# Kernel optimization log

Measured on AMD Instinct MI355X. Metric: run time of the kernel, lower is better.

Reference implementation:

```python
import jax, jax.numpy as jnp
import numpy as np

N_NODES = 50000
N_EDGES = 600000
IN_DIM = 128
HID = 128
OUT_DIM = 2
N_GRAPHS = 64
EPS = 1e-12  # F.normalize default eps


def setup_inputs() -> dict:
    key = jax.random.key(0)
    ks = jax.random.split(key, 16)
    s = 0.05
    x = jax.random.normal(ks[0], (N_NODES, IN_DIM), jnp.float32)
    edge_index = jax.random.randint(ks[1], (2, N_EDGES), 0, N_NODES, dtype=jnp.int32)
    batch = jnp.sort(jax.random.randint(ks[2], (N_NODES,), 0, N_GRAPHS, dtype=jnp.int32))
    # GraphSage layer 0: lin (IN->HID), agg_lin (IN+HID -> HID)
    lin_w0 = jax.random.normal(ks[3], (IN_DIM, HID), jnp.float32) * s
    lin_b0 = jnp.zeros((HID,), jnp.float32)
    agg_w0 = jax.random.normal(ks[4], (HID + IN_DIM, HID), jnp.float32) * s
    agg_b0 = jnp.zeros((HID,), jnp.float32)
    # GraphSage layer 1: lin (HID->HID), agg_lin (2*HID -> HID)
    lin_w1 = jax.random.normal(ks[5], (HID, HID), jnp.float32) * s
    lin_b1 = jnp.zeros((HID,), jnp.float32)
    agg_w1 = jax.random.normal(ks[6], (2 * HID, HID), jnp.float32) * s
    agg_b1 = jnp.zeros((HID,), jnp.float32)
    # post_mp: Linear(HID,HID) -> Dropout -> Linear(HID,OUT)
    mp_w1 = jax.random.normal(ks[7], (HID, HID), jnp.float32) * s
    mp_b1 = jnp.zeros((HID,), jnp.float32)
    mp_w2 = jax.random.normal(ks[8], (HID, OUT_DIM), jnp.float32) * s
    mp_b2 = jnp.zeros((OUT_DIM,), jnp.float32)
    return dict(x=x, edge_index=edge_index, batch=batch,
                lin_w0=lin_w0, lin_b0=lin_b0, agg_w0=agg_w0, agg_b0=agg_b0,
                lin_w1=lin_w1, lin_b1=lin_b1, agg_w1=agg_w1, agg_b1=agg_b1,
                mp_w1=mp_w1, mp_b1=mp_b1, mp_w2=mp_w2, mp_b2=mp_b2)


def sage_layer(x, lin_w, lin_b, agg_w, agg_b, src, dst, num_nodes):
    # message: ReLU(Linear(x_j)) gathered along source nodes  [E, HID]
    msg = jax.nn.relu(x[src] @ lin_w + lin_b)
    # aggr='mean' scatter to target nodes
    summed = jax.ops.segment_sum(msg, dst, num_segments=num_nodes)
    deg = jax.ops.segment_sum(jnp.ones((src.shape[0], 1), x.dtype), dst,
                              num_segments=num_nodes)
    agg = summed / jnp.maximum(deg, 1.0)
    # update: ReLU(Linear([aggr, x])) then L2-normalize rows
    h = jax.nn.relu(jnp.concatenate([agg, x], axis=-1) @ agg_w + agg_b)
    norm = jnp.sqrt(jnp.sum(h * h, axis=1, keepdims=True))
    return h / jnp.maximum(norm, EPS)


def reference(x, edge_index, batch,
              lin_w0, lin_b0, agg_w0, agg_b0,
              lin_w1, lin_b1, agg_w1, agg_b1,
              mp_w1, mp_b1, mp_w2, mp_b2):
    src, dst = edge_index[0], edge_index[1]
    n = x.shape[0]
    h = sage_layer(x, lin_w0, lin_b0, agg_w0, agg_b0, src, dst, n)
    # F.relu is a no-op on the non-negative normalized output; dropout p=0 -> identity
    h = sage_layer(h, lin_w1, lin_b1, agg_w1, agg_b1, src, dst, n)
    # global max pool over graphs
    pooled = jax.ops.segment_max(h, batch, num_segments=N_GRAPHS)
    pooled = jnp.where(jnp.isfinite(pooled), pooled, 0.0)  # guard empty graphs
    # post_mp: Linear -> Dropout(identity) -> Linear
    z = (pooled @ mp_w1 + mp_b1) @ mp_w2 + mp_b2
    return jax.nn.log_softmax(z, axis=1)
```

## Files before the change

kernel.cpp:

```cpp
#include <hip/hip_runtime.h>

__device__ __forceinline__ float bf2f(ushort u) {
    union { uint i; float f; } c; c.i = ((uint)u) << 16; return c.f;
}
__device__ __forceinline__ float bf2lo(uint v) {
    union { uint i; float f; } c; c.i = v << 16; return c.f;
}
__device__ __forceinline__ float bf2hi(uint v) {
    union { uint i; float f; } c; c.i = v & 0xffff0000u; return c.f;
}
__device__ __forceinline__ ushort f2bf(float f) {
    union { float f; uint i; } c; c.f = f;
    uint b = c.i;
    uint r = (b + 0x7fffu + ((b >> 16) & 1u)) >> 16;
    return (ushort)r;
}

typedef __bf16 v8bf __attribute__((ext_vector_type(8)));
typedef float  v4f  __attribute__((ext_vector_type(4)));

__global__ __launch_bounds__(256) void sniff_kernel(const uint* __restrict__ words, int* __restrict__ flag) {
    __shared__ int s[256];
    int t = threadIdx.x;
    int bad = 0;
    for (int i = t; i < 2048; i += 256) {
        uint w = words[i];
        uint exp = (w >> 7) & 0xffu;
        if (exp >= 143u) bad++;
    }
    s[t] = bad;
    __syncthreads();
    for (int o = 128; o; o >>= 1) {
        if (t < o) s[t] += s[t + o];
        __syncthreads();
    }
    if (t == 0) *flag = (s[0] > 64) ? 1 : 0;
}

__device__ __forceinline__ ushort load_conv(const void* src, int i, int isf32) {
    return isf32 ? f2bf(((const float*)src)[i]) : ((const ushort*)src)[i];
}

__global__ __launch_bounds__(256) void convert_x8(const void* __restrict__ src, ushort* __restrict__ dst,
                                                  int n, const int* __restrict__ flag) {
    int idx = blockIdx.x * 256 + threadIdx.x;
    int base = idx * 8;
    if (base + 8 <= n) {
        if (*flag) {
            const float4* s4 = (const float4*)src;
            float4 a = s4[idx * 2], b = s4[idx * 2 + 1];
            union { ushort u[8]; uint4 v; } o;
            o.u[0] = f2bf(a.x); o.u[1] = f2bf(a.y); o.u[2] = f2bf(a.z); o.u[3] = f2bf(a.w);
            o.u[4] = f2bf(b.x); o.u[5] = f2bf(b.y); o.u[6] = f2bf(b.z); o.u[7] = f2bf(b.w);
            *(uint4*)(dst + base) = o.v;
        } else {
            *(uint4*)(dst + base) = ((const uint4*)src)[idx];
        }
    } else {
        int isf = *flag;
        for (int i = base; i < n; i++) dst[i] = load_conv(src, i, isf);
    }
}

struct SmallSrcs { const void* p[8]; };
__global__ __launch_bounds__(256) void prep_weights(
    const void* __restrict__ w0, const void* __restrict__ wa0,
    const void* __restrict__ w1, const void* __restrict__ wa1,
    ushort* __restrict__ t0, ushort* __restrict__ ta0,
    ushort* __restrict__ t1, ushort* __restrict__ ta1,
    SmallSrcs s, ushort* __restrict__ smalldst,
    const int* __restrict__ flag) {
    int idx = blockIdx.x * 256 + threadIdx.x;
    if (idx < 98304) {
        const void* W; ushort* T; int K; int local;
        if (idx < 16384)      { W = w0;  T = t0;  K = 128; local = idx; }
        else if (idx < 49152) { W = wa0; T = ta0; K = 256; local = idx - 16384; }
        else if (idx < 65536) { W = w1;  T = t1;  K = 128; local = idx - 49152; }
        else                  { W = wa1; T = ta1; K = 256; local = idx - 65536; }
        ushort v = load_conv(W, local, *flag);
        int k = local >> 7;
        int n = local & 127;
        T[(size_t)n * K + k] = v;
    } else {
        int si = idx - 98304;
        if (si >= 17282) return;
        const int offs[9] = {0, 128, 256, 384, 512, 16896, 17024, 17280, 17282};
        int seg = 0;
        while (si >= offs[seg + 1]) seg++;
        smalldst[si] = load_conv(s.p[seg], si - offs[seg], *flag);
    }
}

__global__ __launch_bounds__(256) void count_deg(const int* __restrict__ dst, int* __restrict__ deg, int E) {
    int i = blockIdx.x * 256 + threadIdx.x;
    if (i < E) atomicAdd(&deg[dst[i]], 1);
}

#define SCAN_CHUNK 1024

__global__ __launch_bounds__(256) void chunk_sum_kernel(const int* __restrict__ deg,
                                                        int* __restrict__ csums, int n) {
    __shared__ int s[256];
    int t = threadIdx.x;
    int base = blockIdx.x * SCAN_CHUNK + t * 4;
    int v = 0;
    if (base + 4 <= n) {
        int4 q = *(const int4*)(deg + base);
        v = q.x + q.y + q.z + q.w;
    } else {
        for (int i = base; i < n; i++) v += deg[i];
    }
    s[t] = v;
    __syncthreads();
    for (int o = 128; o; o >>= 1) {
        if (t < o) s[t] += s[t + o];
        __syncthreads();
    }
    if (t == 0) csums[blockIdx.x] = s[0];
}

__global__ __launch_bounds__(256) void scan_phase2(const int* __restrict__ deg,
                                                   const int* __restrict__ csums,
                                                   int* __restrict__ rowptr, int* __restrict__ cursor,
                                                   int n) {
    __shared__ int red[256];
    int t = threadIdx.x, b = blockIdx.x;
    int v = 0;
    for (int i = t; i < b; i += 256) v += csums[i];
    red[t] = v;
    __syncthreads();
    for (int o = 128; o; o >>= 1) {
        if (t < o) red[t] += red[t + o];
        __syncthreads();
    }
    int chunkOff = red[0];
    __syncthreads();
    int base = b * SCAN_CHUNK + t * 4;
    int d0 = 0, d1 = 0, d2 = 0, d3 = 0;
    if (base + 4 <= n) {
        int4 q = *(const int4*)(deg + base);
        d0 = q.x; d1 = q.y; d2 = q.z; d3 = q.w;
    } else {
        if (base < n)     d0 = deg[base];
        if (base + 1 < n) d1 = deg[base + 1];
        if (base + 2 < n) d2 = deg[base + 2];
        if (base + 3 < n) d3 = deg[base + 3];
    }
    int s4 = d0 + d1 + d2 + d3;
    red[t] = s4;
    __syncthreads();
    for (int o = 1; o < 256; o <<= 1) {
        int u = (t >= o) ? red[t - o] : 0;
        __syncthreads();
        red[t] += u;
        __syncthreads();
    }
    int run = chunkOff + red[t] - s4;
    if (base < n)     { rowptr[base]     = run; cursor[base]     = run; run += d0; }
    if (base + 1 < n) { rowptr[base + 1] = run; cursor[base + 1] = run; run += d1; }
    if (base + 2 < n) { rowptr[base + 2] = run; cursor[base + 2] = run; run += d2; }
    if (base + 3 < n) { rowptr[base + 3] = run; cursor[base + 3] = run; run += d3; }
    if (n >= base && n < base + 4) rowptr[n] = run;
}

__global__ __launch_bounds__(256) void fill_kernel(const int* __restrict__ src, const int* __restrict__ dst,
                                                   int* __restrict__ cursor, int* __restrict__ csr_src, int E) {
    int i = blockIdx.x * 256 + threadIdx.x;
    if (i < E) {
        int pos = atomicAdd(&cursor[dst[i]], 1);
        csr_src[pos] = src[i];
    }
}

template <int NSTAGE, bool NORM, bool POOL>
__global__ __launch_bounds__(256) void gemm_kernel(
    const ushort* __restrict__ A0, const ushort* __restrict__ A1,
    const ushort* __restrict__ Bt, const ushort* __restrict__ bias,
    ushort* __restrict__ Cout, int M,
    const int* __restrict__ batchv, int* __restrict__ pooled) {
    __shared__ __bf16 As[128 * 72];
    __shared__ __bf16 Bs[128 * 72];
    __shared__ int PoolLoc[POOL ? 8 * 128 : 1];
    const int t = threadIdx.x;
    const int w = t >> 6, lane = t & 63, ln = lane & 15, q = lane >> 4;
    const int blockRow = blockIdx.x * 128;
    const int K = NSTAGE * 128;

    if (POOL) {
        for (int i = t; i < 8 * 128; i += 256) PoolLoc[i] = 0;
    }

    v4f acc[2][8];
#pragma unroll
    for (int i = 0; i < 2; i++)
#pragma unroll
        for (int j = 0; j < 8; j++) acc[i][j] = (v4f){0.f, 0.f, 0.f, 0.f};

    for (int kc = 0; kc < K; kc += 64) {
        const ushort* Ap = (kc < 128) ? A0 : A1;
        int kin = kc & 127;
#pragma unroll
        for (int i = 0; i < 4; i++) {
            int c = i * 256 + t;
            int row = c >> 3, c8 = c & 7;
            int grow = blockRow + row; if (grow >= M) grow = M - 1;
            *(uint4*)&As[row * 72 + c8 * 8] = *(const uint4*)(Ap + (size_t)grow * 128 + kin + c8 * 8);
            *(uint4*)&Bs[row * 72 + c8 * 8] = *(const uint4*)(Bt + (size_t)row * K + kc + c8 * 8);
        }
        __syncthreads();
#pragma unroll
        for (int k0 = 0; k0 < 64; k0 += 32) {
            v8bf a0 = *(const v8bf*)&As[(w * 32 + ln) * 72 + k0 + q * 8];
            v8bf a1 = *(const v8bf*)&As[(w * 32 + 16 + ln) * 72 + k0 + q * 8];
#pragma unroll
            for (int nt = 0; nt < 8; nt++) {
                v8bf b = *(const v8bf*)&Bs[(nt * 16 + ln) * 72 + k0 + q * 8];
                acc[0][nt] = __builtin_amdgcn_mfma_f32_16x16x32_bf16(a0, b, acc[0][nt], 0, 0, 0);
                acc[1][nt] = __builtin_amdgcn_mfma_f32_16x16x32_bf16(a1, b, acc[1][nt], 0, 0, 0);
            }
        }
        __syncthreads();
    }

    float biasf[8];
#pragma unroll
    for (int nt = 0; nt < 8; nt++) biasf[nt] = bf2f(bias[nt * 16 + ln]);

    const int minB = POOL ? batchv[blockRow < M ? blockRow : M - 1] : 0;

#pragma unroll
    for (int mt = 0; mt < 2; mt++) {
        float v[8][4];
#pragma unroll
        for (int nt = 0; nt < 8; nt++)
#pragma unroll
            for (int r = 0; r < 4; r++) {
                float x = acc[mt][nt][r] + biasf[nt];
                v[nt][r] = x > 0.f ? x : 0.f;
            }
        float inv[4];
        if (NORM) {
#pragma unroll
            for (int r = 0; r < 4; r++) {
                float p = 0.f;
#pragma unroll
                for (int nt = 0; nt < 8; nt++) p += v[nt][r] * v[nt][r];
                p += __shfl_xor(p, 1);
                p += __shfl_xor(p, 2);
                p += __shfl_xor(p, 4);
                p += __shfl_xor(p, 8);
                inv[r] = 1.0f / fmaxf(sqrtf(p), 1e-12f);
            }
        }
        int rowbase = blockRow + w * 32 + mt * 16 + q * 4;
#pragma unroll
        for (int r = 0; r < 4; r++) {
            int grow = rowbase + r;
            if (grow < M) {
                if (POOL) {
                    int b = batchv[grow];
                    int rel = b - minB;
#pragma unroll
                    for (int nt = 0; nt < 8; nt++) {
                        float x = v[nt][r] * inv[r];
                        int xi = __float_as_int(x);
                        if (rel < 8) atomicMax(&PoolLoc[rel * 128 + nt * 16 + ln], xi);
                        else         atomicMax(&pooled[b * 128 + nt * 16 + ln], xi);
                    }
                } else {
#pragma unroll
                    for (int nt = 0; nt < 8; nt++) {
                        float x = NORM ? v[nt][r] * inv[r] : v[nt][r];
                        Cout[(size_t)grow * 128 + nt * 16 + ln] = f2bf(x);
                    }
                }
            }
        }
    }

    if (POOL) {
        __syncthreads();
        int lastRow = blockRow + 127; if (lastRow >= M) lastRow = M - 1;
        int span = batchv[lastRow] - minB + 1;
        if (span > 8) span = 8;
        for (int i = t; i < span * 128; i += 256) {
            int vv = PoolLoc[i];
            if (vv != 0) atomicMax(&pooled[(minB + (i >> 7)) * 128 + (i & 127)], vv);
        }
    }
}

__global__ __launch_bounds__(256) void aggregate_kernel(
    const ushort* __restrict__ msg, const int* __restrict__ rowptr,
    const int* __restrict__ csr_src, ushort* __restrict__ agg, int n) {
    int wid = (int)((blockIdx.x * 256u + threadIdx.x) >> 6);
    int lane = threadIdx.x & 63;
    int sub = lane >> 4;
    int l16 = lane & 15;
    if (wid >= n) return;
    int start = rowptr[wid], end = rowptr[wid + 1];
    float a[8] = {0.f, 0.f, 0.f, 0.f, 0.f, 0.f, 0.f, 0.f};
#pragma unroll 2
    for (int j = start + sub; j < end; j += 4) {
        int s = csr_src[j];
        uint4 v = *(const uint4*)(msg + (size_t)s * 128 + l16 * 8);
        a[0] += bf2lo(v.x); a[1] += bf2hi(v.x);
        a[2] += bf2lo(v.y); a[3] += bf2hi(v.y);
        a[4] += bf2lo(v.z); a[5] += bf2hi(v.z);
        a[6] += bf2lo(v.w); a[7] += bf2hi(v.w);
    }
#pragma unroll
    for (int i = 0; i < 8; i++) {
        a[i] += __shfl_xor(a[i], 16);
        a[i] += __shfl_xor(a[i], 32);
    }
    if (sub == 0) {
        float inv = 1.0f / fmaxf((float)(end - start), 1.0f);
        union { ushort u[8]; uint4 v; } o;
#pragma unroll
        for (int i = 0; i < 8; i++) o.u[i] = f2bf(a[i] * inv);
        *(uint4*)(agg + (size_t)wid * 128 + l16 * 8) = o.v;
    }
}

__global__ __launch_bounds__(256) void final_kernel(const float* __restrict__ pooled,
                                                    const ushort* __restrict__ small,
                                                    void* __restrict__ out, int G,
                                                    const int* __restrict__ flag) {
    __shared__ float P[128];
    __shared__ float Thalf[128];
    __shared__ float T[128];
    __shared__ float R0[128], R1[128];
    const ushort* w1 = small + 512;
    const ushort* b1 = small + 16896;
    const ushort* w2 = small + 17024;
    const ushort* b2 = small + 17280;
    int g = blockIdx.x;
    int t = threadIdx.x;
    int j = t & 127, half = t >> 7;
    if (t < 128) P[t] = pooled[g * 128 + t];
    __syncthreads();
    float acc = 0.f;
    int k0 = half * 64;
#pragma unroll 8
    for (int k = k0; k < k0 + 64; k++) acc += P[k] * bf2f(w1[k * 128 + j]);
    if (half == 0) Thalf[j] = acc;
    __syncthreads();
    if (half == 1) T[j] = Thalf[j] + acc + bf2f(b1[j]);
    __syncthreads();
    if (t < 128) {
        float tv = T[t];
        R0[t] = tv * bf2f(w2[t * 2]);
        R1[t] = tv * bf2f(w2[t * 2 + 1]);
    }
    __syncthreads();
    for (int o = 64; o; o >>= 1) {
        if (t < o) { R0[t] += R0[t + o]; R1[t] += R1[t + o]; }
        __syncthreads();
    }
    if (t == 0) {
        float z0 = R0[0] + bf2f(b2[0]);
        float z1 = R1[0] + bf2f(b2[1]);
        float m = fmaxf(z0, z1);
        float l = m + logf(expf(z0 - m) + expf(z1 - m));
        float o0 = z0 - l, o1 = z1 - l;
        if (*flag) {
            ((float*)out)[2 * g]     = o0;
            ((float*)out)[2 * g + 1] = o1;
        } else {
            ((ushort*)out)[2 * g]     = f2bf(o0);
            ((ushort*)out)[2 * g + 1] = f2bf(o1);
        }
    }
}

extern "C" void kernel_launch(void* const* d_in, const int* in_sizes, int n_in,
                              void* d_out, int out_size, void* d_ws, size_t ws_size,
                              hipStream_t stream) {
    const void* x      = d_in[0];
    const int*  ei     = (const int*)d_in[1];
    const int*  batch  = (const int*)d_in[2];

    const int N = in_sizes[0] / 128;
    const int E = in_sizes[1] / 2;
    const int G = out_size / 2;
    const int* srcIdx = ei;
    const int* dstIdx = ei + E;

    char* ws = (char*)d_ws;
    size_t off = 0;
    auto alloc = [&](size_t bytes) -> void* {
        off = (off + 255) & ~(size_t)255;
        void* p = ws + off;
        off += bytes;
        return p;
    };
    int*    flag    = (int*)alloc(4);
    int*    deg     = (int*)alloc((size_t)N * 4);
    int*    rowptr  = (int*)alloc((size_t)(N + 1) * 4);
    int*    cursor  = (int*)alloc((size_t)N * 4);
    int*    csr_src = (int*)alloc((size_t)E * 4);
    int*    csums   = (int*)alloc(((size_t)N / SCAN_CHUNK + 2) * 4);
    ushort* Wt0     = (ushort*)alloc(128 * 128 * 2);
    ushort* WtA0    = (ushort*)alloc(256 * 128 * 2);
    ushort* Wt1     = (ushort*)alloc(128 * 128 * 2);
    ushort* WtA1    = (ushort*)alloc(256 * 128 * 2);
    ushort* small   = (ushort*)alloc(17282 * 2);
    ushort* xb      = (ushort*)alloc((size_t)N * 128 * 2);
    ushort* msg     = (ushort*)alloc((size_t)N * 128 * 2);
    ushort* agg     = (ushort*)alloc((size_t)N * 128 * 2);
    ushort* h0      = (ushort*)alloc((size_t)N * 128 * 2);
    int*    pooled  = (int*)alloc((size_t)G * 128 * 4);

    sniff_kernel<<<1, 256, 0, stream>>>((const uint*)x, flag);
    convert_x8<<<(N * 128 + 2047) / 2048, 256, 0, stream>>>(x, xb, N * 128, flag);
    SmallSrcs ss;
    ss.p[0] = d_in[4];  ss.p[1] = d_in[6];  ss.p[2] = d_in[8];  ss.p[3] = d_in[10];
    ss.p[4] = d_in[11]; ss.p[5] = d_in[12]; ss.p[6] = d_in[13]; ss.p[7] = d_in[14];
    prep_weights<<<452, 256, 0, stream>>>(d_in[3], d_in[5], d_in[7], d_in[9],
                                          Wt0, WtA0, Wt1, WtA1, ss, small, flag);

    hipMemsetAsync(deg, 0, (size_t)N * 4, stream);
    hipMemsetAsync(pooled, 0, (size_t)G * 128 * 4, stream);
    int eb = (E + 255) / 256;
    count_deg<<<eb, 256, 0, stream>>>(dstIdx, deg, E);
    int nchunks = (N + SCAN_CHUNK - 1) / SCAN_CHUNK;
    chunk_sum_kernel<<<nchunks, 256, 0, stream>>>(deg, csums, N);
    scan_phase2<<<N / SCAN_CHUNK + 1, 256, 0, stream>>>(deg, csums, rowptr, cursor, N);
    fill_kernel<<<eb, 256, 0, stream>>>(srcIdx, dstIdx, cursor, csr_src, E);

    int gb = (N + 127) / 128;
    int ab = (N + 3) / 4;

    gemm_kernel<1, false, false><<<gb, 256, 0, stream>>>(xb, xb, Wt0, small + 0, msg, N, nullptr, nullptr);
    aggregate_kernel<<<ab, 256, 0, stream>>>(msg, rowptr, csr_src, agg, N);
    gemm_kernel<2, true, false><<<gb, 256, 0, stream>>>(agg, xb, WtA0, small + 128, h0, N, nullptr, nullptr);

    gemm_kernel<1, false, false><<<gb, 256, 0, stream>>>(h0, h0, Wt1, small + 256, msg, N, nullptr, nullptr);
    aggregate_kernel<<<ab, 256, 0, stream>>>(msg, rowptr, csr_src, agg, N);
    gemm_kernel<2, true, true><<<gb, 256, 0, stream>>>(agg, h0, WtA1, small + 384, nullptr, N, batch, pooled);

    final_kernel<<<G, 256, 0, stream>>>((const float*)pooled, small, d_out, G, flag);
}
```

Before: 282.7 us.

## Fuse layer-1 message GEMM into layer-0 update GEMM and merge prep kernels

```diff
diff --git a/kernel.cpp b/kernel.cpp
--- a/kernel.cpp
+++ b/kernel.cpp
@@ -41,53 +41,63 @@
     return isf32 ? f2bf(((const float*)src)[i]) : ((const ushort*)src)[i];
 }
 
-__global__ __launch_bounds__(256) void convert_x8(const void* __restrict__ src, ushort* __restrict__ dst,
-                                                  int n, const int* __restrict__ flag) {
-    int idx = blockIdx.x * 256 + threadIdx.x;
-    int base = idx * 8;
-    if (base + 8 <= n) {
-        if (*flag) {
-            const float4* s4 = (const float4*)src;
-            float4 a = s4[idx * 2], b = s4[idx * 2 + 1];
-            union { ushort u[8]; uint4 v; } o;
-            o.u[0] = f2bf(a.x); o.u[1] = f2bf(a.y); o.u[2] = f2bf(a.z); o.u[3] = f2bf(a.w);
-            o.u[4] = f2bf(b.x); o.u[5] = f2bf(b.y); o.u[6] = f2bf(b.z); o.u[7] = f2bf(b.w);
-            *(uint4*)(dst + base) = o.v;
-        } else {
-            *(uint4*)(dst + base) = ((const uint4*)src)[idx];
-        }
-    } else {
-        int isf = *flag;
-        for (int i = base; i < n; i++) dst[i] = load_conv(src, i, isf);
-    }
-}
-
 struct SmallSrcs { const void* p[8]; };
-__global__ __launch_bounds__(256) void prep_weights(
+__global__ __launch_bounds__(256) void phaseA(
+    const void* __restrict__ x, ushort* __restrict__ xb, int nx, int nbconv,
     const void* __restrict__ w0, const void* __restrict__ wa0,
     const void* __restrict__ w1, const void* __restrict__ wa1,
     ushort* __restrict__ t0, ushort* __restrict__ ta0,
     ushort* __restrict__ t1, ushort* __restrict__ ta1,
     SmallSrcs s, ushort* __restrict__ smalldst,
+    int* __restrict__ deg, int* __restrict__ pooled, int N, int G,
     const int* __restrict__ flag) {
-    int idx = blockIdx.x * 256 + threadIdx.x;
-    if (idx < 98304) {
-        const void* W; ushort* T; int K; int local;
-        if (idx < 16384)      { W = w0;  T = t0;  K = 128; local = idx; }
-        else if (idx < 49152) { W = wa0; T = ta0; K = 256; local = idx - 16384; }
-        else if (idx < 65536) { W = w1;  T = t1;  K = 128; local = idx - 49152; }
-        else                  { W = wa1; T = ta1; K = 256; local = idx - 65536; }
-        ushort v = load_conv(W, local, *flag);
-        int k = local >> 7;
-        int n = local & 127;
-        T[(size_t)n * K + k] = v;
+    int b = blockIdx.x, t = threadIdx.x;
+    if (b < nbconv) {
+        int idx = b * 256 + t;
+        int base = idx * 8;
+        if (base + 8 <= nx) {
+            if (*flag) {
+                const float4* s4 = (const float4*)x;
+                float4 a = s4[idx * 2], bb = s4[idx * 2 + 1];
+                union { ushort u[8]; uint4 v; } o;
+                o.u[0] = f2bf(a.x); o.u[1] = f2bf(a.y); o.u[2] = f2bf(a.z); o.u[3] = f2bf(a.w);
+                o.u[4] = f2bf(bb.x); o.u[5] = f2bf(bb.y); o.u[6] = f2bf(bb.z); o.u[7] = f2bf(bb.w);
+                *(uint4*)(xb + base) = o.v;
+            } else {
+                *(uint4*)(xb + base) = ((const uint4*)x)[idx];
+            }
+        } else {
+            int isf = *flag;
+            for (int i = base; i < nx; i++) xb[i] = load_conv(x, i, isf);
+        }
+    } else if (b < nbconv + 452) {
+        int idx = (b - nbconv) * 256 + t;
+        if (idx < 98304) {
+            const void* W; ushort* T; int K; int local;
+            if (idx < 16384)      { W = w0;  T = t0;  K = 128; local = idx; }
+            else if (idx < 49152) { W = wa0; T = ta0; K = 256; local = idx - 16384; }
+            else if (idx < 65536) { W = w1;  T = t1;  K = 128; local = idx - 49152; }
+            else                  { W = wa1; T = ta1; K = 256; local = idx - 65536; }
+            ushort v = load_conv(W, local, *flag);
+            int k = local >> 7;
+            int n = local & 127;
+            T[(size_t)n * K + k] = v;
+        } else {
+            int si = idx - 98304;
+            if (si < 17282) {
+                const int offs[9] = {0, 128, 256, 384, 512, 16896, 17024, 17280, 17282};
+                int seg = 0;
+                while (si >= offs[seg + 1]) seg++;
+                smalldst[si] = load_conv(s.p[seg], si - offs[seg], *flag);
+            }
+        }
     } else {
-        int si = idx - 98304;
-        if (si >= 17282) return;
-        const int offs[9] = {0, 128, 256, 384, 512, 16896, 17024, 17280, 17282};
-        int seg = 0;
-        while (si >= offs[seg + 1]) seg++;
-        smalldst[si] = load_conv(s.p[seg], si - offs[seg], *flag);
+        int idx = (b - nbconv - 452) * 256 + t;
+        int nd4 = N >> 2;
+        int4 z = {0, 0, 0, 0};
+        if (idx < nd4) ((int4*)deg)[idx] = z;
+        else if (idx == nd4) { for (int i = nd4 * 4; i < N; i++) deg[i] = 0; }
+        else if (idx - nd4 - 1 < G * 32) ((int4*)pooled)[idx - nd4 - 1] = z;
     }
 }
 
@@ -172,15 +182,19 @@
     }
 }
 
-template <int NSTAGE, bool NORM, bool POOL>
+template <int NSTAGE, bool NORM, bool POOL, bool FUSE>
 __global__ __launch_bounds__(256) void gemm_kernel(
     const ushort* __restrict__ A0, const ushort* __restrict__ A1,
     const ushort* __restrict__ Bt, const ushort* __restrict__ bias,
     ushort* __restrict__ Cout, int M,
-    const int* __restrict__ batchv, int* __restrict__ pooled) {
-    __shared__ __bf16 As[128 * 72];
-    __shared__ __bf16 Bs[128 * 72];
+    const int* __restrict__ batchv, int* __restrict__ pooled,
+    const ushort* __restrict__ Bt2, const ushort* __restrict__ bias2,
+    ushort* __restrict__ Mout) {
+    constexpr int LDSN = FUSE ? (128 * 136 + 128 * 72) : (2 * 128 * 72);
+    __shared__ __bf16 lds[LDSN];
     __shared__ int PoolLoc[POOL ? 8 * 128 : 1];
+    __bf16* As = lds;
+    __bf16* Bs = lds + 128 * 72;
     const int t = threadIdx.x;
     const int w = t >> 6, lane = t & 63, ln = lane & 15, q = lane >> 4;
     const int blockRow = blockIdx.x * 128;
@@ -227,6 +241,8 @@
     for (int nt = 0; nt < 8; nt++) biasf[nt] = bf2f(bias[nt * 16 + ln]);
 
     const int minB = POOL ? batchv[blockRow < M ? blockRow : M - 1] : 0;
+    __bf16* Hs = lds;
+    ushort* HsU = (ushort*)Hs;
 
 #pragma unroll
     for (int mt = 0; mt < 2; mt++) {
@@ -252,12 +268,12 @@
                 inv[r] = 1.0f / fmaxf(sqrtf(p), 1e-12f);
             }
         }
-        int rowbase = blockRow + w * 32 + mt * 16 + q * 4;
+        int rowloc = w * 32 + mt * 16 + q * 4;
 #pragma unroll
         for (int r = 0; r < 4; r++) {
-            int grow = rowbase + r;
-            if (grow < M) {
-                if (POOL) {
+            int grow = blockRow + rowloc + r;
+            if (POOL) {
+                if (grow < M) {
                     int b = batchv[grow];
                     int rel = b - minB;
 #pragma unroll
@@ -267,12 +283,14 @@
                         if (rel < 8) atomicMax(&PoolLoc[rel * 128 + nt * 16 + ln], xi);
                         else         atomicMax(&pooled[b * 128 + nt * 16 + ln], xi);
                     }
-                } else {
-#pragma unroll
-                    for (int nt = 0; nt < 8; nt++) {
-                        float x = NORM ? v[nt][r] * inv[r] : v[nt][r];
-                        Cout[(size_t)grow * 128 + nt * 16 + ln] = f2bf(x);
-                    }
+                }
+            } else {
+#pragma unroll
+                for (int nt = 0; nt < 8; nt++) {
+                    float x = NORM ? v[nt][r] * inv[r] : v[nt][r];
+                    ushort xb = f2bf(x);
+                    if (grow < M) Cout[(size_t)grow * 128 + nt * 16 + ln] = xb;
+                    if (FUSE) HsU[(rowloc + r) * 136 + nt * 16 + ln] = xb;
                 }
             }
         }
@@ -286,6 +304,56 @@
         for (int i = t; i < span * 128; i += 256) {
             int vv = PoolLoc[i];
             if (vv != 0) atomicMax(&pooled[(minB + (i >> 7)) * 128 + (i & 127)], vv);
+        }
+    }
+
+    if (FUSE) {
+        __bf16* Bs2 = lds + 128 * 136;
+        v4f acc2[2][8];
+#pragma unroll
+        for (int i = 0; i < 2; i++)
+#pragma unroll
+            for (int j = 0; j < 8; j++) acc2[i][j] = (v4f){0.f, 0.f, 0.f, 0.f};
+
+        for (int kc = 0; kc < 128; kc += 64) {
+#pragma unroll
+            for (int i = 0; i < 4; i++) {
+                int c = i * 256 + t;
+                int row = c >> 3, c8 = c & 7;
+                *(uint4*)&Bs2[row * 72 + c8 * 8] = *(const uint4*)(Bt2 + (size_t)row * 128 + kc + c8 * 8);
+            }
+            __syncthreads();
+#pragma unroll
+            for (int k0 = 0; k0 < 64; k0 += 32) {
+                v8bf a0 = *(const v8bf*)&Hs[(w * 32 + ln) * 136 + kc + k0 + q * 8];
+                v8bf a1 = *(const v8bf*)&Hs[(w * 32 + 16 + ln) * 136 + kc + k0 + q * 8];
+#pragma unroll
+                for (int nt = 0; nt < 8; nt++) {
+                    v8bf b = *(const v8bf*)&Bs2[(nt * 16 + ln) * 72 + k0 + q * 8];
+                    acc2[0][nt] = __builtin_amdgcn_mfma_f32_16x16x32_bf16(a0, b, acc2[0][nt], 0, 0, 0);
+                    acc2[1][nt] = __builtin_amdgcn_mfma_f32_16x16x32_bf16(a1, b, acc2[1][nt], 0, 0, 0);
+                }
+            }
+            __syncthreads();
+        }
+
+        float biasf2[8];
+#pragma unroll
+        for (int nt = 0; nt < 8; nt++) biasf2[nt] = bf2f(bias2[nt * 16 + ln]);
+#pragma unroll
+        for (int mt = 0; mt < 2; mt++) {
+            int rowbase = blockRow + w * 32 + mt * 16 + q * 4;
+#pragma unroll
+            for (int r = 0; r < 4; r++) {
+                int grow = rowbase + r;
+                if (grow < M) {
+#pragma unroll
+                    for (int nt = 0; nt < 8; nt++) {
+                        float x = acc2[mt][nt][r] + biasf2[nt];
+                        Mout[(size_t)grow * 128 + nt * 16 + ln] = f2bf(x > 0.f ? x : 0.f);
+                    }
+                }
+            }
         }
     }
 }
@@ -413,32 +481,37 @@
     int*    pooled  = (int*)alloc((size_t)G * 128 * 4);
 
     sniff_kernel<<<1, 256, 0, stream>>>((const uint*)x, flag);
-    convert_x8<<<(N * 128 + 2047) / 2048, 256, 0, stream>>>(x, xb, N * 128, flag);
+
     SmallSrcs ss;
     ss.p[0] = d_in[4];  ss.p[1] = d_in[6];  ss.p[2] = d_in[8];  ss.p[3] = d_in[10];
     ss.p[4] = d_in[11]; ss.p[5] = d_in[12]; ss.p[6] = d_in[13]; ss.p[7] = d_in[14];
-    prep_weights<<<452, 256, 0, stream>>>(d_in[3], d_in[5], d_in[7], d_in[9],
-                                          Wt0, WtA0, Wt1, WtA1, ss, small, flag);
-
-    hipMemsetAsync(deg, 0, (size_t)N * 4, stream);
-    hipMemsetAsync(pooled, 0, (size_t)G * 128 * 4, stream);
+    int nbconv = (N * 128 + 2047) / 2048;
+    int nbzero = ((N / 4 + 1 + G * 32) + 255) / 256;
+    phaseA<<<nbconv + 452 + nbzero, 256, 0, stream>>>(
+        x, xb, N * 128, nbconv,
+        d_in[3], d_in[5], d_in[7], d_in[9],
+        Wt0, WtA0, Wt1, WtA1, ss, small, deg, pooled, N, G, flag);
+
+    int gb = (N + 127) / 128;
+    int ab = (N + 3) / 4;
     int eb = (E + 255) / 256;
+
+    gemm_kernel<1, false, false, false><<<gb, 256, 0, stream>>>(
+        xb, xb, Wt0, small + 0, msg, N, nullptr, nullptr, nullptr, nullptr, nullptr);
+
     count_deg<<<eb, 256, 0, stream>>>(dstIdx, deg, E);
     int nchunks = (N + SCAN_CHUNK - 1) / SCAN_CHUNK;
     chunk_sum_kernel<<<nchunks, 256, 0, stream>>>(deg, csums, N);
     scan_phase2<<<N / SCAN_CHUNK + 1, 256, 0, stream>>>(deg, csums, rowptr, cursor, N);
     fill_kernel<<<eb, 256, 0, stream>>>(srcIdx, dstIdx, cursor, csr_src, E);
 
-    int gb = (N + 127) / 128;
-    int ab = (N + 3) / 4;
-
-    gemm_kernel<1, false, false><<<gb, 256, 0, stream>>>(xb, xb, Wt0, small + 0, msg, N, nullptr, nullptr);
     aggregate_kernel<<<ab, 256, 0, stream>>>(msg, rowptr, csr_src, agg, N);
-    gemm_kernel<2, true, false><<<gb, 256, 0, stream>>>(agg, xb, WtA0, small + 128, h0, N, nullptr, nullptr);
-
-    gemm_kernel<1, false, false><<<gb, 256, 0, stream>>>(h0, h0, Wt1, small + 256, msg, N, nullptr, nullptr);
+    gemm_kernel<2, true, false, true><<<gb, 256, 0, stream>>>(
+        agg, xb, WtA0, small + 128, h0, N, nullptr, nullptr, Wt1, small + 256, msg);
+
     aggregate_kernel<<<ab, 256, 0, stream>>>(msg, rowptr, csr_src, agg, N);
-    gemm_kernel<2, true, true><<<gb, 256, 0, stream>>>(agg, h0, WtA1, small + 384, nullptr, N, batch, pooled);
+    gemm_kernel<2, true, true, false><<<gb, 256, 0, stream>>>(
+        agg, h0, WtA1, small + 384, nullptr, N, batch, pooled, nullptr, nullptr, nullptr);
 
     final_kernel<<<G, 256, 0, stream>>>((const float*)pooled, small, d_out, G, flag);
 }
```

Result: faster. 273.5 us (-3.3%).
